# Kernel optimization log

Hardware: AMD Instinct MI355X
Metric: run time of the kernel (lower is better)

The kernel has to match this reference:

```python
import jax, jax.numpy as jnp
import numpy as np

B, R, F = 64, 196, 2048   # batch, regions, feature_dim
E, H, A = 512, 512, 512   # embed_dim, hidden_dim, attn_dim
V, L = 12000, 24          # vocab, seq_len


def setup_inputs() -> dict:
    key = jax.random.key(0)
    ks = jax.random.split(key, 16)
    s = lambda *d: 1.0 / np.sqrt(d[-1])
    inp = {
        'image_feats': jax.random.normal(ks[0], (B, R, F), jnp.float32),
        'caption_in': jax.random.randint(ks[1], (B, L), 0, V, jnp.int64),
        'emb_table': jax.random.normal(ks[2], (V, E), jnp.float32) * 0.02,
        'W_init_h': jax.random.normal(ks[3], (H, F), jnp.float32) * s(F),
        'b_init_h': jnp.zeros((H,), jnp.float32),
        'W_init_c': jax.random.normal(ks[4], (H, F), jnp.float32) * s(F),
        'b_init_c': jnp.zeros((H,), jnp.float32),
        'W_ih': jax.random.normal(ks[5], (4 * H, E + F), jnp.float32) * s(E + F),
        'b_ih': jnp.zeros((4 * H,), jnp.float32),
        'W_hh': jax.random.normal(ks[6], (4 * H, H), jnp.float32) * s(H),
        'b_hh': jnp.zeros((4 * H,), jnp.float32),
        'W_featp': jax.random.normal(ks[7], (A, F), jnp.float32) * s(F),
        'b_featp': jnp.zeros((A,), jnp.float32),
        'W_hidp': jax.random.normal(ks[8], (A, H), jnp.float32) * s(H),
        'b_hidp': jnp.zeros((A,), jnp.float32),
        'W_score': jax.random.normal(ks[9], (1, A), jnp.float32) * s(A),
        'b_score': jnp.zeros((1,), jnp.float32),
        'W_out': jax.random.normal(ks[10], (V, H), jnp.float32) * s(H),
        'b_out': jnp.zeros((V,), jnp.float32),
    }
    return inp


def _forward(image_feats, caption_in, emb_table, W_init_h, b_init_h, W_init_c,
             b_init_c, W_ih, b_ih, W_hh, b_hh, W_featp, b_featp, W_hidp,
             b_hidp, W_score, b_score, W_out, b_out):
    # init hidden state from mean image features
    mean_feats = image_feats.mean(axis=1)                      # (B, F)
    h0 = mean_feats @ W_init_h.T + b_init_h                    # (B, H)
    c0 = mean_feats @ W_init_c.T + b_init_c                    # (B, H)

    embeddings = emb_table[caption_in]                         # (B, L, E)  (dropout in eval mode = identity)

    # feature projection is constant over timesteps -> hoist out of the scan
    feat_proj = jnp.einsum('brf,af->bra', image_feats, W_featp) + b_featp  # (B, R, A)

    def step(carry, emb_t):
        h, c = carry
        # additive attention
        hid_proj = h @ W_hidp.T + b_hidp                       # (B, A)
        energy = jnp.tanh(feat_proj + hid_proj[:, None, :])    # (B, R, A)
        scores = jnp.einsum('bra,a->br', energy, W_score[0]) + b_score[0]
        alpha = jax.nn.softmax(scores, axis=1)                 # (B, R)
        context = jnp.einsum('br,brf->bf', alpha, image_feats) # (B, F)
        # LSTM cell (PyTorch gate order: i, f, g, o)
        x = jnp.concatenate([emb_t, context], axis=1)          # (B, E+F)
        gates = x @ W_ih.T + b_ih + h @ W_hh.T + b_hh          # (B, 4H)
        i, f, g, o = jnp.split(gates, 4, axis=1)
        c_new = jax.nn.sigmoid(f) * c + jax.nn.sigmoid(i) * jnp.tanh(g)
        h_new = jax.nn.sigmoid(o) * jnp.tanh(c_new)
        out = h_new @ W_out.T + b_out                          # (B, V)
        return (h_new, c_new), (out, alpha)

    emb_t = jnp.swapaxes(embeddings, 0, 1)                     # (L, B, E)
    _, (preds, alphas) = jax.lax.scan(step, (h0, c0), emb_t)
    predictions = jnp.swapaxes(preds, 0, 1)                    # (B, L, V)
    all_alphas = jnp.swapaxes(alphas, 0, 1)                    # (B, L, R)
    return predictions, all_alphas


def reference(image_feats, caption_in, emb_table, W_init_h, b_init_h, W_init_c,
              b_init_c, W_ih, b_ih, W_hh, b_hh, W_featp, b_featp, W_hidp,
              b_hidp, W_score, b_score, W_out, b_out):
    return _forward(image_feats, caption_in, emb_table, W_init_h, b_init_h,
                    W_init_c, b_init_c, W_ih, b_ih, W_hh, b_hh, W_featp,
                    b_featp, W_hidp, b_hidp, W_score, b_score, W_out, b_out)
```

## Files before the change

kernel.cpp:

```cpp
#include <hip/hip_runtime.h>

#define B_ 64
#define R_ 196
#define F_ 2048
#define E_ 512
#define H_ 512
#define A_ 512
#define V_ 12000
#define L_ 24

typedef __attribute__((ext_vector_type(8))) short bf16x8;
typedef __attribute__((ext_vector_type(4))) float f32x4;
typedef unsigned short ush;

__device__ __forceinline__ float fast_tanh(float x) {
    float t = __expf(2.f * x);
    return 1.f - 2.f / (t + 1.f);
}
__device__ __forceinline__ float fast_sig(float x) {
    return 1.f / (1.f + __expf(-x));
}
__device__ __forceinline__ ush f2bf(float x) {
    unsigned int u = __float_as_uint(x);
    return (ush)((u + 0x7fffu + ((u >> 16) & 1u)) >> 16);
}
__device__ __forceinline__ float bf2f(ush b) {
    return __uint_as_float(((unsigned int)b) << 16);
}

#define LROW 40

template<int SPLIT, int CMAP, bool NFAST>
__global__ __launch_bounds__(512) void gemm_big128(
    const ush* __restrict__ Ah, const ush* __restrict__ Al, int lda,
    const ush* __restrict__ Wh, const ush* __restrict__ Wl, int ldw,
    const float* __restrict__ bias, void* __restrict__ Cv,
    int ldc, int N, int K)
{
    constexpr int SMEM_BYTES = (SPLIT == 3) ? 61440 : 30720;
    __shared__ __align__(16) char smem[SMEM_BYTES];
    ush* sAh = (ush*)smem;
    ush* sBh = (ush*)(smem + 10240);
    ush* sAl = (ush*)(smem + 30720);
    ush* sBl = (ush*)(smem + 40960);

    const int tid = threadIdx.x;
    const int lane = tid & 63, w = tid >> 6;
    const int mw = w >> 2, nw = w & 3;

    const int nbx = gridDim.x, nby = gridDim.y;
    const int nwg = nbx * nby;
    const int orig = blockIdx.x + nbx * blockIdx.y;
    const int q = nwg >> 3, r = nwg & 7;
    const int xcd = orig & 7, idx = orig >> 3;
    const int lin = (xcd < r ? xcd * (q + 1) : r * (q + 1) + (xcd - r) * q) + idx;
    int bx, by;
    if constexpr (NFAST) { by = lin % nby; bx = lin / nby; }
    else                 { bx = lin % nbx; by = lin / nbx; }
    const int mtile = bx * 128;
    const int ntile = by * 256;

    const int fr = lane & 15, kg = (lane >> 4) * 8;
    const int arow = tid >> 2, aq = (tid & 3) * 8;

    f32x4 acc[4][4];
    #pragma unroll
    for (int mf = 0; mf < 4; ++mf)
        #pragma unroll
        for (int nf = 0; nf < 4; ++nf) acc[mf][nf] = {0.f, 0.f, 0.f, 0.f};

    const uint4 zv = make_uint4(0u, 0u, 0u, 0u);

    for (int kb = 0; kb < K; kb += 32) {
        uint4 a_h = *(const uint4*)(Ah + (size_t)(mtile + arow) * lda + kb + aq);
        uint4 a_l;
        uint4 b_h[2], b_l[2];
        #pragma unroll
        for (int p = 0; p < 2; ++p) {
            const int row = ntile + arow + 128 * p;
            b_h[p] = (row < N) ? *(const uint4*)(Wh + (size_t)row * ldw + kb + aq) : zv;
        }
        if constexpr (SPLIT == 3) {
            a_l = *(const uint4*)(Al + (size_t)(mtile + arow) * lda + kb + aq);
            #pragma unroll
            for (int p = 0; p < 2; ++p) {
                const int row = ntile + arow + 128 * p;
                b_l[p] = (row < N) ? *(const uint4*)(Wl + (size_t)row * ldw + kb + aq) : zv;
            }
        }

        __syncthreads();
        *(uint4*)(sAh + arow * LROW + aq) = a_h;
        #pragma unroll
        for (int p = 0; p < 2; ++p)
            *(uint4*)(sBh + (arow + 128 * p) * LROW + aq) = b_h[p];
        if constexpr (SPLIT == 3) {
            *(uint4*)(sAl + arow * LROW + aq) = a_l;
            #pragma unroll
            for (int p = 0; p < 2; ++p)
                *(uint4*)(sBl + (arow + 128 * p) * LROW + aq) = b_l[p];
        }
        __syncthreads();

        bf16x8 bh[4], bl[4];
        #pragma unroll
        for (int nf = 0; nf < 4; ++nf) {
            bh[nf] = *(const bf16x8*)(sBh + (nw * 64 + nf * 16 + fr) * LROW + kg);
            if constexpr (SPLIT == 3)
                bl[nf] = *(const bf16x8*)(sBl + (nw * 64 + nf * 16 + fr) * LROW + kg);
        }
        #pragma unroll
        for (int mf = 0; mf < 4; ++mf) {
            const bf16x8 ah = *(const bf16x8*)(sAh + (mw * 64 + mf * 16 + fr) * LROW + kg);
            if constexpr (SPLIT == 3) {
                const bf16x8 al = *(const bf16x8*)(sAl + (mw * 64 + mf * 16 + fr) * LROW + kg);
                #pragma unroll
                for (int nf = 0; nf < 4; ++nf) {
                    acc[mf][nf] = __builtin_amdgcn_mfma_f32_16x16x32_bf16(ah, bh[nf], acc[mf][nf], 0, 0, 0);
                    acc[mf][nf] = __builtin_amdgcn_mfma_f32_16x16x32_bf16(ah, bl[nf], acc[mf][nf], 0, 0, 0);
                    acc[mf][nf] = __builtin_amdgcn_mfma_f32_16x16x32_bf16(al, bh[nf], acc[mf][nf], 0, 0, 0);
                }
            } else {
                #pragma unroll
                for (int nf = 0; nf < 4; ++nf)
                    acc[mf][nf] = __builtin_amdgcn_mfma_f32_16x16x32_bf16(ah, bh[nf], acc[mf][nf], 0, 0, 0);
            }
        }
    }

    #pragma unroll
    for (int nf = 0; nf < 4; ++nf) {
        const int nn = ntile + nw * 64 + nf * 16 + fr;
        if (nn < N) {
            const float bv = bias ? bias[nn] : 0.f;
            #pragma unroll
            for (int mf = 0; mf < 4; ++mf) {
                #pragma unroll
                for (int rr = 0; rr < 4; ++rr) {
                    const int m = mtile + mw * 64 + mf * 16 + (lane >> 4) * 4 + rr;
                    const float v = acc[mf][nf][rr] + bv;
                    if constexpr (CMAP == 1)
                        ((ush*)Cv)[(size_t)m * ldc + nn] = f2bf(v);
                    else if constexpr (CMAP == 2) {
                        float* dst = (float*)Cv + (size_t)(m & 63) * (L_ * V_)
                                   + (size_t)(m >> 6) * V_ + nn;
                        __builtin_nontemporal_store(v, dst);
                    } else
                        ((float*)Cv)[(size_t)m * ldc + nn] = v;
                }
            }
        }
    }
}

template<int SPLIT, int CMAP, bool NFAST, int NF>
__global__ __launch_bounds__(256) void gemm_big(
    const ush* __restrict__ Ah, const ush* __restrict__ Al, int lda,
    const ush* __restrict__ Wh, const ush* __restrict__ Wl, int ldw,
    const float* __restrict__ bias, void* __restrict__ Cv,
    int ldc, int N, int K)
{
    constexpr int ABYTES = 64 * LROW * 2;
    constexpr int BBYTES = 64 * NF * LROW * 2;
    constexpr int SMEM_BYTES = (SPLIT == 3) ? 2 * (ABYTES + BBYTES) : (ABYTES + BBYTES);
    __shared__ __align__(16) char smem[SMEM_BYTES];
    ush* sAh = (ush*)smem;
    ush* sBh = (ush*)(smem + ABYTES);
    ush* sAl = (ush*)(smem + ABYTES + BBYTES);
    ush* sBl = (ush*)(smem + 2 * ABYTES + BBYTES);

    const int tid = threadIdx.x;
    const int lane = tid & 63, w = tid >> 6;

    const int nbx = gridDim.x, nby = gridDim.y;
    const int nwg = nbx * nby;
    int lin = blockIdx.x + nbx * blockIdx.y;
    if ((nwg & 7) == 0) {
        const int q = nwg >> 3;
        lin = (lin & 7) * q + (lin >> 3);
    }
    int bx, by;
    if constexpr (NFAST) { by = lin % nby; bx = lin / nby; }
    else                 { bx = lin % nbx; by = lin / nbx; }
    const int mtile = bx * 64;
    const int ntile = by * (64 * NF);

    const int fr = lane & 15, kg = (lane >> 4) * 8;
    const int arow = tid >> 2, aq = (tid & 3) * 8;

    f32x4 acc[4][NF];
    #pragma unroll
    for (int mf = 0; mf < 4; ++mf)
        #pragma unroll
        for (int nf = 0; nf < NF; ++nf) acc[mf][nf] = {0.f, 0.f, 0.f, 0.f};

    const uint4 zv = make_uint4(0u, 0u, 0u, 0u);

    for (int kb = 0; kb < K; kb += 32) {
        uint4 a_h = *(const uint4*)(Ah + (size_t)(mtile + arow) * lda + kb + aq);
        uint4 a_l;
        uint4 b_h[NF], b_l[NF];
        #pragma unroll
        for (int p = 0; p < NF; ++p) {
            const int row = ntile + arow + 64 * p;
            b_h[p] = (row < N) ? *(const uint4*)(Wh + (size_t)row * ldw + kb + aq) : zv;
        }
        if constexpr (SPLIT == 3) {
            a_l = *(const uint4*)(Al + (size_t)(mtile + arow) * lda + kb + aq);
            #pragma unroll
            for (int p = 0; p < NF; ++p) {
                const int row = ntile + arow + 64 * p;
                b_l[p] = (row < N) ? *(const uint4*)(Wl + (size_t)row * ldw + kb + aq) : zv;
            }
        }

        __syncthreads();
        *(uint4*)(sAh + arow * LROW + aq) = a_h;
        #pragma unroll
        for (int p = 0; p < NF; ++p)
            *(uint4*)(sBh + (arow + 64 * p) * LROW + aq) = b_h[p];
        if constexpr (SPLIT == 3) {
            *(uint4*)(sAl + arow * LROW + aq) = a_l;
            #pragma unroll
            for (int p = 0; p < NF; ++p)
                *(uint4*)(sBl + (arow + 64 * p) * LROW + aq) = b_l[p];
        }
        __syncthreads();

        bf16x8 bh[NF], bl[NF];
        #pragma unroll
        for (int nf = 0; nf < NF; ++nf) {
            bh[nf] = *(const bf16x8*)(sBh + (w * (16 * NF) + nf * 16 + fr) * LROW + kg);
            if constexpr (SPLIT == 3)
                bl[nf] = *(const bf16x8*)(sBl + (w * (16 * NF) + nf * 16 + fr) * LROW + kg);
        }
        #pragma unroll
        for (int mf = 0; mf < 4; ++mf) {
            const bf16x8 ah = *(const bf16x8*)(sAh + (mf * 16 + fr) * LROW + kg);
            if constexpr (SPLIT == 3) {
                const bf16x8 al = *(const bf16x8*)(sAl + (mf * 16 + fr) * LROW + kg);
                #pragma unroll
                for (int nf = 0; nf < NF; ++nf) {
                    acc[mf][nf] = __builtin_amdgcn_mfma_f32_16x16x32_bf16(ah, bh[nf], acc[mf][nf], 0, 0, 0);
                    acc[mf][nf] = __builtin_amdgcn_mfma_f32_16x16x32_bf16(ah, bl[nf], acc[mf][nf], 0, 0, 0);
                    acc[mf][nf] = __builtin_amdgcn_mfma_f32_16x16x32_bf16(al, bh[nf], acc[mf][nf], 0, 0, 0);
                }
            } else {
                #pragma unroll
                for (int nf = 0; nf < NF; ++nf)
                    acc[mf][nf] = __builtin_amdgcn_mfma_f32_16x16x32_bf16(ah, bh[nf], acc[mf][nf], 0, 0, 0);
            }
        }
    }

    #pragma unroll
    for (int nf = 0; nf < NF; ++nf) {
        const int nn = ntile + w * (16 * NF) + nf * 16 + fr;
        if (nn < N) {
            const float bv = bias ? bias[nn] : 0.f;
            #pragma unroll
            for (int mf = 0; mf < 4; ++mf) {
                #pragma unroll
                for (int rr = 0; rr < 4; ++rr) {
                    const int m = mtile + mf * 16 + (lane >> 4) * 4 + rr;
                    const float v = acc[mf][nf][rr] + bv;
                    if constexpr (CMAP == 1)
                        ((ush*)Cv)[(size_t)m * ldc + nn] = f2bf(v);
                    else
                        ((float*)Cv)[(size_t)m * ldc + nn] = v;
                }
            }
        }
    }
}

__global__ __launch_bounds__(256) void gemm_gates(
    const ush* __restrict__ Ah0, const ush* __restrict__ Al0, int lda0, int k0,
    const ush* __restrict__ Ah1, const ush* __restrict__ Al1, int lda1,
    const ush* __restrict__ Wh, const ush* __restrict__ Wl, int ldw,
    float* __restrict__ C, int ldc, long zstride, int kChunk)
{
    __shared__ ush sAh[64 * LROW];
    __shared__ ush sBh[64 * LROW];
    __shared__ ush sAl[64 * LROW];
    __shared__ ush sBl[64 * LROW];

    const int tid = threadIdx.x;
    const int ntile = blockIdx.x * 64;
    const int kStart = blockIdx.z * kChunk;
    const int lane = tid & 63, w = tid >> 6;
    const int lrow = tid >> 2;
    const int lcol = (tid & 3) * 8;
    const int nrow = ntile + lrow;

    f32x4 acc[4];
    #pragma unroll
    for (int f = 0; f < 4; ++f) acc[f] = {0.f, 0.f, 0.f, 0.f};

    const int fr = lane & 15;
    const int kg = (lane >> 4) * 8;

    for (int kb = kStart; kb < kStart + kChunk; kb += 32) {
        const ush *ph, *pl; int lda, loc;
        if (kb < k0) { ph = Ah0; pl = Al0; lda = lda0; loc = kb; }
        else         { ph = Ah1; pl = Al1; lda = lda1; loc = kb - k0; }

        uint4 a_h = *(const uint4*)(ph + (size_t)lrow * lda + loc + lcol);
        uint4 b_h = *(const uint4*)(Wh + (size_t)nrow * ldw + kb + lcol);
        uint4 a_l = *(const uint4*)(pl + (size_t)lrow * lda + loc + lcol);
        uint4 b_l = *(const uint4*)(Wl + (size_t)nrow * ldw + kb + lcol);

        __syncthreads();
        *(uint4*)(sAh + lrow * LROW + lcol) = a_h;
        *(uint4*)(sBh + lrow * LROW + lcol) = b_h;
        *(uint4*)(sAl + lrow * LROW + lcol) = a_l;
        *(uint4*)(sBl + lrow * LROW + lcol) = b_l;
        __syncthreads();

        const bf16x8 bh = *(const bf16x8*)(sBh + (16 * w + fr) * LROW + kg);
        const bf16x8 bl = *(const bf16x8*)(sBl + (16 * w + fr) * LROW + kg);

        #pragma unroll
        for (int f = 0; f < 4; ++f) {
            const bf16x8 ah = *(const bf16x8*)(sAh + (16 * f + fr) * LROW + kg);
            const bf16x8 al = *(const bf16x8*)(sAl + (16 * f + fr) * LROW + kg);
            acc[f] = __builtin_amdgcn_mfma_f32_16x16x32_bf16(ah, bh, acc[f], 0, 0, 0);
            acc[f] = __builtin_amdgcn_mfma_f32_16x16x32_bf16(ah, bl, acc[f], 0, 0, 0);
            acc[f] = __builtin_amdgcn_mfma_f32_16x16x32_bf16(al, bh, acc[f], 0, 0, 0);
        }
    }

    const int n = ntile + 16 * w + (lane & 15);
    float* Cz = C + (size_t)blockIdx.z * zstride;
    #pragma unroll
    for (int f = 0; f < 4; ++f)
        #pragma unroll
        for (int rr = 0; rr < 4; ++rr) {
            const int m = 16 * f + (lane >> 4) * 4 + rr;
            Cz[(size_t)m * ldc + n] = acc[f][rr];
        }
}

__global__ __launch_bounds__(256) void prep_feats(
    const float* __restrict__ feats, ush* __restrict__ fbh,
    ush* __restrict__ mh, ush* __restrict__ ml)
{
    const int fs = blockIdx.x;
    const int b  = blockIdx.y;
    const int f = fs * 512 + threadIdx.x * 2;
    const float2* fp = (const float2*)(feats + (size_t)b * R_ * F_ + f);
    ush* fo = fbh + (size_t)b * R_ * F_ + f;
    float sx = 0.f, sy = 0.f;
    for (int r = 0; r < R_; ++r) {
        const float2 v = fp[(size_t)r * (F_ / 2)];
        sx += v.x; sy += v.y;
        ushort2 u; u.x = f2bf(v.x); u.y = f2bf(v.y);
        *(ushort2*)(fo + (size_t)r * F_) = u;
    }
    const float s = 1.f / (float)R_;
    sx *= s; sy *= s;
    const size_t mi = (size_t)b * F_ + f;
    const ush hx = f2bf(sx); mh[mi] = hx;     ml[mi] = f2bf(sx - bf2f(hx));
    const ush hy = f2bf(sy); mh[mi + 1] = hy; ml[mi + 1] = f2bf(sy - bf2f(hy));
}

__global__ __launch_bounds__(256) void gather_split(
    const float* __restrict__ emb, const int* __restrict__ cap,
    ush* __restrict__ eh, ush* __restrict__ el)
{
    const int idx = blockIdx.x * 256 + threadIdx.x;
    const int bt = idx >> 7, j = idx & 127;
    const int tok = cap[bt];
    const float4 v = reinterpret_cast<const float4*>(emb)[(size_t)tok * (E_ / 4) + j];
    const float a[4] = {v.x, v.y, v.z, v.w};
    #pragma unroll
    for (int c = 0; c < 4; ++c) {
        const ush hi = f2bf(a[c]);
        eh[idx * 4 + c] = hi;
        el[idx * 4 + c] = f2bf(a[c] - bf2f(hi));
    }
}

__global__ __launch_bounds__(256) void split_kernel(
    const float* __restrict__ in, ush* __restrict__ hi, ush* __restrict__ lo, int n4)
{
    for (int i = blockIdx.x * 256 + threadIdx.x; i < n4; i += gridDim.x * 256) {
        const float4 v = reinterpret_cast<const float4*>(in)[i];
        const float a[4] = {v.x, v.y, v.z, v.w};
        #pragma unroll
        for (int c = 0; c < 4; ++c) {
            const ush h = f2bf(a[c]);
            hi[i * 4 + c] = h;
            if (lo) lo[i * 4 + c] = f2bf(a[c] - bf2f(h));
        }
    }
}

__global__ __launch_bounds__(256) void prep_wih(
    const float* __restrict__ W_ih, const float* __restrict__ W_hh,
    ush* __restrict__ wxh, ush* __restrict__ wxl,
    ush* __restrict__ wg2h, ush* __restrict__ wg2l)
{
    const int nrow = blockIdx.x;
    for (int k = threadIdx.x; k < E_; k += 256) {
        const float v = W_ih[(size_t)nrow * (E_ + F_) + k];
        const ush h = f2bf(v);
        wxh[(size_t)nrow * E_ + k] = h;
        wxl[(size_t)nrow * E_ + k] = f2bf(v - bf2f(h));
    }
    for (int k = threadIdx.x; k < F_ + H_; k += 256) {
        const float v = (k < F_) ? W_ih[(size_t)nrow * (E_ + F_) + E_ + k]
                                 : W_hh[(size_t)nrow * H_ + (k - F_)];
        const ush h = f2bf(v);
        wg2h[(size_t)nrow * (F_ + H_) + k] = h;
        wg2l[(size_t)nrow * (F_ + H_) + k] = f2bf(v - bf2f(h));
    }
}

__global__ __launch_bounds__(256) void transpose512(
    const float* __restrict__ in, float* __restrict__ out)
{
    const int idx = blockIdx.x * 256 + threadIdx.x;
    const int k = idx >> 9, a = idx & 511;
    out[idx] = in[(size_t)a * 512 + k];
    (void)k;
}

__global__ __launch_bounds__(256) void init_reduce(
    const float* __restrict__ initp, const float* __restrict__ b_init_h,
    const float* __restrict__ b_init_c, float* __restrict__ h0f,
    float* __restrict__ c, ush* __restrict__ h_hi, ush* __restrict__ h_lo)
{
    const int idx = blockIdx.x * 256 + threadIdx.x;
    const int b = idx >> 10, n = idx & 1023;
    float s = 0.f;
    #pragma unroll
    for (int z = 0; z < 8; ++z)
        s += initp[(size_t)z * (B_ * 1024) + (size_t)b * 1024 + n];
    if (n < 512) {
        s += b_init_h[n];
        h0f[b * H_ + n] = s;
        const ush hi = f2bf(s);
        h_hi[b * H_ + n] = hi;
        h_lo[b * H_ + n] = f2bf(s - bf2f(hi));
    } else {
        s += b_init_c[n - 512];
        c[b * H_ + (n - 512)] = s;
    }
}

template<bool ATT>
__global__ __launch_bounds__(512) void step_kernel(
    const float* __restrict__ gparts, const float* __restrict__ egates,
    const float* __restrict__ b_ih, const float* __restrict__ b_hh,
    float* __restrict__ c, const float* __restrict__ h0f,
    ush* __restrict__ h_hi, ush* __restrict__ h_lo,
    ush* __restrict__ hall_hi, ush* __restrict__ hall_lo,
    const float* __restrict__ whpT, const float* __restrict__ b_hidp,
    const ush* __restrict__ fpb, const float* __restrict__ W_score,
    const float* __restrict__ b_score,
    float* __restrict__ alpha, float* __restrict__ alph_out, int t)
{
    __shared__ float sh_h[H_];
    __shared__ float sh_hp[A_];
    __shared__ float sh_ws[A_];
    __shared__ float sh_sc[200];
    __shared__ float red[2];
    const int tid = threadIdx.x;
    const int b = blockIdx.x;
    const int n = tid;

    float hh;
    if (t > 0) {
        const float* eg = egates + ((size_t)b * L_ + (t - 1)) * 2048;
        float gi = b_ih[n] + b_hh[n] + eg[n];
        float gf = b_ih[n + 512] + b_hh[n + 512] + eg[n + 512];
        float gg = b_ih[n + 1024] + b_hh[n + 1024] + eg[n + 1024];
        float go = b_ih[n + 1536] + b_hh[n + 1536] + eg[n + 1536];
        #pragma unroll
        for (int z = 0; z < 8; ++z) {
            const float* gz = gparts + (size_t)z * B_ * 2048 + (size_t)b * 2048;
            gi += gz[n]; gf += gz[n + 512]; gg += gz[n + 1024]; go += gz[n + 1536];
        }
        const float cc = fast_sig(gf) * c[b * H_ + n] + fast_sig(gi) * fast_tanh(gg);
        hh = fast_sig(go) * fast_tanh(cc);
        c[b * H_ + n] = cc;
        const ush hi = f2bf(hh);
        const ush lo = f2bf(hh - bf2f(hi));
        h_hi[b * H_ + n] = hi;
        h_lo[b * H_ + n] = lo;
        const size_t hidx = ((size_t)(t - 1) * B_ + b) * H_ + n;
        hall_hi[hidx] = hi;
        hall_lo[hidx] = lo;
    } else {
        hh = h0f[b * H_ + n];
    }
    if constexpr (!ATT) return;

    sh_h[n] = hh;
    sh_ws[n] = W_score[n];
    __syncthreads();

    {
        float a0 = 0.f, a1 = 0.f, a2 = 0.f, a3 = 0.f;
        #pragma unroll 4
        for (int k = 0; k < H_; k += 4) {
            a0 = fmaf(sh_h[k + 0], whpT[(size_t)(k + 0) * A_ + tid], a0);
            a1 = fmaf(sh_h[k + 1], whpT[(size_t)(k + 1) * A_ + tid], a1);
            a2 = fmaf(sh_h[k + 2], whpT[(size_t)(k + 2) * A_ + tid], a2);
            a3 = fmaf(sh_h[k + 3], whpT[(size_t)(k + 3) * A_ + tid], a3);
        }
        sh_hp[tid] = (a0 + a1) + (a2 + a3) + b_hidp[tid];
    }
    __syncthreads();

    const int lane = tid & 63, wid = tid >> 6;
    for (int r = wid; r < R_; r += 8) {
        const ushort2* row = reinterpret_cast<const ushort2*>(fpb + ((size_t)b * R_ + r) * A_);
        float acc = 0.f;
        #pragma unroll
        for (int j = 0; j < 4; ++j) {
            const ushort2 u = row[lane + 64 * j];
            const int a = 2 * (lane + 64 * j);
            acc += fast_tanh(bf2f(u.x) + sh_hp[a]) * sh_ws[a];
            acc += fast_tanh(bf2f(u.y) + sh_hp[a + 1]) * sh_ws[a + 1];
        }
        for (int off = 32; off > 0; off >>= 1) acc += __shfl_down(acc, off);
        if (lane == 0) sh_sc[r] = acc + b_score[0];
    }
    __syncthreads();

    if (tid < 64) {
        float m = -1e30f;
        for (int r = tid; r < R_; r += 64) m = fmaxf(m, sh_sc[r]);
        for (int off = 32; off > 0; off >>= 1) m = fmaxf(m, __shfl_xor(m, off));
        float s = 0.f;
        for (int r = tid; r < R_; r += 64) s += __expf(sh_sc[r] - m);
        for (int off = 32; off > 0; off >>= 1) s += __shfl_xor(s, off);
        if (tid == 0) { red[0] = m; red[1] = 1.f / s; }
    }
    __syncthreads();
    const float m = red[0], is = red[1];
    if (tid < R_) {
        const float av = __expf(sh_sc[tid] - m) * is;
        alpha[b * R_ + tid] = av;
        alph_out[((size_t)b * L_ + t) * R_ + tid] = av;
    }
}

__global__ __launch_bounds__(256) void ctx_kernel(
    const ush* __restrict__ fbh, const float* __restrict__ alpha,
    ush* __restrict__ ctx_hi, ush* __restrict__ ctx_lo)
{
    __shared__ float sa[R_];
    const int tid = threadIdx.x;
    const int fs = blockIdx.x;
    const int b = blockIdx.y;
    if (tid < R_) sa[tid] = alpha[b * R_ + tid];
    __syncthreads();

    const int f0 = fs * 512 + tid * 2;
    const ush* fp = fbh + (size_t)b * R_ * F_ + f0;
    float cx = 0.f, cy = 0.f;
    #pragma unroll 4
    for (int r = 0; r < R_; ++r) {
        const float a = sa[r];
        const ushort2 u = *(const ushort2*)(fp + (size_t)r * F_);
        cx = fmaf(a, bf2f(u.x), cx); cy = fmaf(a, bf2f(u.y), cy);
    }
    const size_t ci = (size_t)b * F_ + f0;
    const ush hx = f2bf(cx);
    ctx_hi[ci] = hx; ctx_lo[ci] = f2bf(cx - bf2f(hx));
    const ush hy = f2bf(cy);
    ctx_hi[ci + 1] = hy; ctx_lo[ci + 1] = f2bf(cy - bf2f(hy));
}

extern "C" void kernel_launch(void* const* d_in, const int* in_sizes, int n_in,
                              void* d_out, int out_size, void* d_ws, size_t ws_size,
                              hipStream_t stream)
{
    const float* feats    = (const float*)d_in[0];
    const int*   cap      = (const int*)  d_in[1];
    const float* emb      = (const float*)d_in[2];
    const float* W_init_h = (const float*)d_in[3];
    const float* b_init_h = (const float*)d_in[4];
    const float* W_init_c = (const float*)d_in[5];
    const float* b_init_c = (const float*)d_in[6];
    const float* W_ih     = (const float*)d_in[7];
    const float* b_ih     = (const float*)d_in[8];
    const float* W_hh     = (const float*)d_in[9];
    const float* b_hh     = (const float*)d_in[10];
    const float* W_featp  = (const float*)d_in[11];
    const float* b_featp  = (const float*)d_in[12];
    const float* W_hidp   = (const float*)d_in[13];
    const float* b_hidp   = (const float*)d_in[14];
    const float* W_score  = (const float*)d_in[15];
    const float* b_score  = (const float*)d_in[16];
    const float* W_out    = (const float*)d_in[17];
    const float* b_out    = (const float*)d_in[18];

    float* pred     = (float*)d_out;
    float* alph_out = pred + (size_t)B_ * L_ * V_;

    char* p = (char*)d_ws;
    auto alloc = [&](size_t bytes) { char* q = p; p += (bytes + 255) & ~(size_t)255; return q; };

    ush*   fpb    = (ush*)  alloc((size_t)B_ * R_ * A_ * 2);
    ush*   eh     = (ush*)  alloc((size_t)B_ * L_ * E_ * 2);
    ush*   el     = (ush*)  alloc((size_t)B_ * L_ * E_ * 2);
    ush*   mh     = (ush*)  alloc((size_t)B_ * F_ * 2);
    ush*   ml     = (ush*)  alloc((size_t)B_ * F_ * 2);
    ush*   fbh    = (ush*)  alloc((size_t)B_ * R_ * F_ * 2);
    ush*   wfp_h  = (ush*)  alloc((size_t)A_ * F_ * 2);
    ush*   wiH    = (ush*)  alloc((size_t)1024 * F_ * 2);
    ush*   wiL    = (ush*)  alloc((size_t)1024 * F_ * 2);
    ush*   wxh    = (ush*)  alloc((size_t)2048 * E_ * 2);
    ush*   wxl    = (ush*)  alloc((size_t)2048 * E_ * 2);
    ush*   wg2h   = (ush*)  alloc((size_t)2048 * (F_ + H_) * 2);
    ush*   wg2l   = (ush*)  alloc((size_t)2048 * (F_ + H_) * 2);
    ush*   woh    = (ush*)  alloc((size_t)V_ * H_ * 2);
    ush*   wol    = (ush*)  alloc((size_t)V_ * H_ * 2);
    float* whpT   = (float*)alloc((size_t)H_ * A_ * 4);
    float* egates = (float*)alloc((size_t)B_ * L_ * 2048 * 4);
    float* h0f    = (float*)alloc((size_t)B_ * H_ * 4);
    float* c      = (float*)alloc((size_t)B_ * H_ * 4);
    ush*   h_hi   = (ush*)  alloc((size_t)B_ * H_ * 2);
    ush*   h_lo   = (ush*)  alloc((size_t)B_ * H_ * 2);
    ush*   hallh  = (ush*)  alloc((size_t)L_ * B_ * H_ * 2);
    ush*   halll  = (ush*)  alloc((size_t)L_ * B_ * H_ * 2);
    ush*   ctx_hi = (ush*)  alloc((size_t)B_ * F_ * 2);
    ush*   ctx_lo = (ush*)  alloc((size_t)B_ * F_ * 2);
    float* alpha  = (float*)alloc((size_t)B_ * R_ * 4);
    float* gparts = (float*)alloc((size_t)8 * B_ * 2048 * 4);
    float* initp  = (float*)alloc((size_t)8 * B_ * 1024 * 4);

    prep_feats<<<dim3(4, B_), 256, 0, stream>>>(feats, fbh, mh, ml);
    gather_split<<<768, 256, 0, stream>>>(emb, cap, eh, el);
    split_kernel<<<2048, 256, 0, stream>>>(W_out, woh, wol, V_ * H_ / 4);
    split_kernel<<<512, 256, 0, stream>>>(W_init_h, wiH, wiL, H_ * F_ / 4);
    split_kernel<<<512, 256, 0, stream>>>(W_init_c, wiH + (size_t)512 * F_,
                                          wiL + (size_t)512 * F_, H_ * F_ / 4);
    split_kernel<<<512, 256, 0, stream>>>(W_featp, wfp_h, nullptr, A_ * F_ / 4);
    prep_wih<<<2048, 256, 0, stream>>>(W_ih, W_hh, wxh, wxl, wg2h, wg2l);
    transpose512<<<1024, 256, 0, stream>>>(W_hidp, whpT);

    gemm_gates<<<dim3(16, 1, 8), 256, 0, stream>>>(
        mh, ml, F_, F_,
        mh, ml, F_,
        wiH, wiL, F_,
        initp, 1024, (long)B_ * 1024, F_ / 8);
    init_reduce<<<256, 256, 0, stream>>>(initp, b_init_h, b_init_c, h0f, c, h_hi, h_lo);

    gemm_big<1, 1, true, 2><<<dim3(196, 4), 256, 0, stream>>>(
        fbh, nullptr, F_, wfp_h, nullptr, F_, b_featp, fpb, A_, A_, F_);

    gemm_big<3, 0, false, 2><<<dim3(24, 16), 256, 0, stream>>>(
        eh, el, E_, wxh, wxl, E_, nullptr, egates, 2048, 2048, E_);

    for (int t = 0; t < L_; ++t) {
        step_kernel<true><<<B_, 512, 0, stream>>>(
            gparts, egates, b_ih, b_hh, c, h0f, h_hi, h_lo, hallh, halll,
            whpT, b_hidp, fpb, W_score, b_score, alpha, alph_out, t);

        ctx_kernel<<<dim3(4, B_), 256, 0, stream>>>(fbh, alpha, ctx_hi, ctx_lo);

        gemm_gates<<<dim3(32, 1, 8), 256, 0, stream>>>(
            ctx_hi, ctx_lo, F_, F_,
            h_hi, h_lo, H_,
            wg2h, wg2l, F_ + H_,
            gparts, 4 * H_, (long)B_ * 4 * H_, (F_ + H_) / 8);
    }

    step_kernel<false><<<B_, 512, 0, stream>>>(
        gparts, egates, b_ih, b_hh, c, h0f, h_hi, h_lo, hallh, halll,
        whpT, b_hidp, fpb, W_score, b_score, alpha, alph_out, L_);

    gemm_big128<3, 2, false><<<dim3(12, 47), 512, 0, stream>>>(
        hallh, halll, H_, woh, wol, H_, b_out, pred, 0, V_, H_);
}
```

Baseline: 2.100 ms.

## Fuse attention step and context reduction into one per-batch kernel

Merges the per-timestep attention/LSTM-update kernel with the context-weighted-sum kernel, launching 4 blocks per batch that each redundantly compute the LSTM cell and attention softmax and then reduce one 512-wide feature slice. The cell state is double-buffered so the redundant blocks do not race on it. The hidden-projection weight is stored as bf16 to halve its reads. A template argument of the feature-projection GEMM launch also changes along with its grid. This removes one launch per timestep and the alpha round trip through global memory, at the cost of 4x redundant attention work per batch.

```diff
diff --git a/kernel.cpp b/kernel.cpp
--- a/kernel.cpp
+++ b/kernel.cpp
@@ -418,18 +418,17 @@
 }
 
 __global__ __launch_bounds__(256) void transpose512(
-    const float* __restrict__ in, float* __restrict__ out)
+    const float* __restrict__ in, ush* __restrict__ out)
 {
     const int idx = blockIdx.x * 256 + threadIdx.x;
     const int k = idx >> 9, a = idx & 511;
-    out[idx] = in[(size_t)a * 512 + k];
-    (void)k;
+    out[idx] = f2bf(in[(size_t)a * 512 + k]);
 }
 
 __global__ __launch_bounds__(256) void init_reduce(
     const float* __restrict__ initp, const float* __restrict__ b_init_h,
     const float* __restrict__ b_init_c, float* __restrict__ h0f,
-    float* __restrict__ c, ush* __restrict__ h_hi, ush* __restrict__ h_lo)
+    float* __restrict__ c0, ush* __restrict__ h_hi, ush* __restrict__ h_lo)
 {
     const int idx = blockIdx.x * 256 + threadIdx.x;
     const int b = idx >> 10, n = idx & 1023;
@@ -445,21 +444,22 @@
         h_lo[b * H_ + n] = f2bf(s - bf2f(hi));
     } else {
         s += b_init_c[n - 512];
-        c[b * H_ + (n - 512)] = s;
+        c0[b * H_ + (n - 512)] = s;
     }
 }
 
 template<bool ATT>
-__global__ __launch_bounds__(512) void step_kernel(
+__global__ __launch_bounds__(512) void step2_kernel(
     const float* __restrict__ gparts, const float* __restrict__ egates,
     const float* __restrict__ b_ih, const float* __restrict__ b_hh,
-    float* __restrict__ c, const float* __restrict__ h0f,
+    float* __restrict__ c2, const float* __restrict__ h0f,
     ush* __restrict__ h_hi, ush* __restrict__ h_lo,
     ush* __restrict__ hall_hi, ush* __restrict__ hall_lo,
-    const float* __restrict__ whpT, const float* __restrict__ b_hidp,
+    const ush* __restrict__ whpT, const float* __restrict__ b_hidp,
     const ush* __restrict__ fpb, const float* __restrict__ W_score,
-    const float* __restrict__ b_score,
-    float* __restrict__ alpha, float* __restrict__ alph_out, int t)
+    const float* __restrict__ b_score, const ush* __restrict__ fbh,
+    ush* __restrict__ ctx_hi, ush* __restrict__ ctx_lo,
+    float* __restrict__ alph_out, int t)
 {
     __shared__ float sh_h[H_];
     __shared__ float sh_hp[A_];
@@ -467,11 +467,14 @@
     __shared__ float sh_sc[200];
     __shared__ float red[2];
     const int tid = threadIdx.x;
-    const int b = blockIdx.x;
+    const int fs = blockIdx.x;
+    const int b = blockIdx.y;
     const int n = tid;
 
     float hh;
     if (t > 0) {
+        const float* c_old = c2 + (size_t)((t - 1) & 1) * B_ * H_;
+        float* c_new = c2 + (size_t)(t & 1) * B_ * H_;
         const float* eg = egates + ((size_t)b * L_ + (t - 1)) * 2048;
         float gi = b_ih[n] + b_hh[n] + eg[n];
         float gf = b_ih[n + 512] + b_hh[n + 512] + eg[n + 512];
@@ -482,16 +485,18 @@
             const float* gz = gparts + (size_t)z * B_ * 2048 + (size_t)b * 2048;
             gi += gz[n]; gf += gz[n + 512]; gg += gz[n + 1024]; go += gz[n + 1536];
         }
-        const float cc = fast_sig(gf) * c[b * H_ + n] + fast_sig(gi) * fast_tanh(gg);
+        const float cc = fast_sig(gf) * c_old[b * H_ + n] + fast_sig(gi) * fast_tanh(gg);
         hh = fast_sig(go) * fast_tanh(cc);
-        c[b * H_ + n] = cc;
-        const ush hi = f2bf(hh);
-        const ush lo = f2bf(hh - bf2f(hi));
-        h_hi[b * H_ + n] = hi;
-        h_lo[b * H_ + n] = lo;
-        const size_t hidx = ((size_t)(t - 1) * B_ + b) * H_ + n;
-        hall_hi[hidx] = hi;
-        hall_lo[hidx] = lo;
+        if (fs == 0) {
+            c_new[b * H_ + n] = cc;
+            const ush hi = f2bf(hh);
+            const ush lo = f2bf(hh - bf2f(hi));
+            h_hi[b * H_ + n] = hi;
+            h_lo[b * H_ + n] = lo;
+            const size_t hidx = ((size_t)(t - 1) * B_ + b) * H_ + n;
+            hall_hi[hidx] = hi;
+            hall_lo[hidx] = lo;
+        }
     } else {
         hh = h0f[b * H_ + n];
     }
@@ -505,10 +510,10 @@
         float a0 = 0.f, a1 = 0.f, a2 = 0.f, a3 = 0.f;
         #pragma unroll 4
         for (int k = 0; k < H_; k += 4) {
-            a0 = fmaf(sh_h[k + 0], whpT[(size_t)(k + 0) * A_ + tid], a0);
-            a1 = fmaf(sh_h[k + 1], whpT[(size_t)(k + 1) * A_ + tid], a1);
-            a2 = fmaf(sh_h[k + 2], whpT[(size_t)(k + 2) * A_ + tid], a2);
-            a3 = fmaf(sh_h[k + 3], whpT[(size_t)(k + 3) * A_ + tid], a3);
+            a0 = fmaf(sh_h[k + 0], bf2f(whpT[(size_t)(k + 0) * A_ + tid]), a0);
+            a1 = fmaf(sh_h[k + 1], bf2f(whpT[(size_t)(k + 1) * A_ + tid]), a1);
+            a2 = fmaf(sh_h[k + 2], bf2f(whpT[(size_t)(k + 2) * A_ + tid]), a2);
+            a3 = fmaf(sh_h[k + 3], bf2f(whpT[(size_t)(k + 3) * A_ + tid]), a3);
         }
         sh_hp[tid] = (a0 + a1) + (a2 + a3) + b_hidp[tid];
     }
@@ -543,36 +548,23 @@
     const float m = red[0], is = red[1];
     if (tid < R_) {
         const float av = __expf(sh_sc[tid] - m) * is;
-        alpha[b * R_ + tid] = av;
-        alph_out[((size_t)b * L_ + t) * R_ + tid] = av;
-    }
-}
-
-__global__ __launch_bounds__(256) void ctx_kernel(
-    const ush* __restrict__ fbh, const float* __restrict__ alpha,
-    ush* __restrict__ ctx_hi, ush* __restrict__ ctx_lo)
-{
-    __shared__ float sa[R_];
-    const int tid = threadIdx.x;
-    const int fs = blockIdx.x;
-    const int b = blockIdx.y;
-    if (tid < R_) sa[tid] = alpha[b * R_ + tid];
+        sh_sc[tid] = av;
+        if (fs == 0) alph_out[((size_t)b * L_ + t) * R_ + tid] = av;
+    }
     __syncthreads();
 
-    const int f0 = fs * 512 + tid * 2;
-    const ush* fp = fbh + (size_t)b * R_ * F_ + f0;
-    float cx = 0.f, cy = 0.f;
-    #pragma unroll 4
-    for (int r = 0; r < R_; ++r) {
-        const float a = sa[r];
-        const ushort2 u = *(const ushort2*)(fp + (size_t)r * F_);
-        cx = fmaf(a, bf2f(u.x), cx); cy = fmaf(a, bf2f(u.y), cy);
-    }
-    const size_t ci = (size_t)b * F_ + f0;
-    const ush hx = f2bf(cx);
-    ctx_hi[ci] = hx; ctx_lo[ci] = f2bf(cx - bf2f(hx));
-    const ush hy = f2bf(cy);
-    ctx_hi[ci + 1] = hy; ctx_lo[ci + 1] = f2bf(cy - bf2f(hy));
+    {
+        const int f0 = fs * 512 + tid;
+        const ush* fp2 = fbh + (size_t)b * R_ * F_ + f0;
+        float cx = 0.f;
+        #pragma unroll 4
+        for (int r = 0; r < R_; ++r)
+            cx = fmaf(sh_sc[r], bf2f(fp2[(size_t)r * F_]), cx);
+        const size_t ci = (size_t)b * F_ + f0;
+        const ush hx = f2bf(cx);
+        ctx_hi[ci] = hx;
+        ctx_lo[ci] = f2bf(cx - bf2f(hx));
+    }
 }
 
 extern "C" void kernel_launch(void* const* d_in, const int* in_sizes, int n_in,
@@ -620,17 +612,16 @@
     ush*   wg2l   = (ush*)  alloc((size_t)2048 * (F_ + H_) * 2);
     ush*   woh    = (ush*)  alloc((size_t)V_ * H_ * 2);
     ush*   wol    = (ush*)  alloc((size_t)V_ * H_ * 2);
-    float* whpT   = (float*)alloc((size_t)H_ * A_ * 4);
+    ush*   whpT   = (ush*)  alloc((size_t)H_ * A_ * 2);
     float* egates = (float*)alloc((size_t)B_ * L_ * 2048 * 4);
     float* h0f    = (float*)alloc((size_t)B_ * H_ * 4);
-    float* c      = (float*)alloc((size_t)B_ * H_ * 4);
+    float* c2     = (float*)alloc((size_t)2 * B_ * H_ * 4);
     ush*   h_hi   = (ush*)  alloc((size_t)B_ * H_ * 2);
     ush*   h_lo   = (ush*)  alloc((size_t)B_ * H_ * 2);
     ush*   hallh  = (ush*)  alloc((size_t)L_ * B_ * H_ * 2);
     ush*   halll  = (ush*)  alloc((size_t)L_ * B_ * H_ * 2);
     ush*   ctx_hi = (ush*)  alloc((size_t)B_ * F_ * 2);
     ush*   ctx_lo = (ush*)  alloc((size_t)B_ * F_ * 2);
-    float* alpha  = (float*)alloc((size_t)B_ * R_ * 4);
     float* gparts = (float*)alloc((size_t)8 * B_ * 2048 * 4);
     float* initp  = (float*)alloc((size_t)8 * B_ * 1024 * 4);
 
@@ -649,20 +640,19 @@
         mh, ml, F_,
         wiH, wiL, F_,
         initp, 1024, (long)B_ * 1024, F_ / 8);
-    init_reduce<<<256, 256, 0, stream>>>(initp, b_init_h, b_init_c, h0f, c, h_hi, h_lo);
-
-    gemm_big<1, 1, true, 2><<<dim3(196, 4), 256, 0, stream>>>(
+    init_reduce<<<256, 256, 0, stream>>>(initp, b_init_h, b_init_c, h0f, c2, h_hi, h_lo);
+
+    gemm_big<1, 1, true, 1><<<dim3(196, 8), 256, 0, stream>>>(
         fbh, nullptr, F_, wfp_h, nullptr, F_, b_featp, fpb, A_, A_, F_);
 
     gemm_big<3, 0, false, 2><<<dim3(24, 16), 256, 0, stream>>>(
         eh, el, E_, wxh, wxl, E_, nullptr, egates, 2048, 2048, E_);
 
     for (int t = 0; t < L_; ++t) {
-        step_kernel<true><<<B_, 512, 0, stream>>>(
-            gparts, egates, b_ih, b_hh, c, h0f, h_hi, h_lo, hallh, halll,
-            whpT, b_hidp, fpb, W_score, b_score, alpha, alph_out, t);
-
-        ctx_kernel<<<dim3(4, B_), 256, 0, stream>>>(fbh, alpha, ctx_hi, ctx_lo);
+        step2_kernel<true><<<dim3(4, B_), 512, 0, stream>>>(
+            gparts, egates, b_ih, b_hh, c2, h0f, h_hi, h_lo, hallh, halll,
+            whpT, b_hidp, fpb, W_score, b_score, fbh, ctx_hi, ctx_lo,
+            alph_out, t);
 
         gemm_gates<<<dim3(32, 1, 8), 256, 0, stream>>>(
             ctx_hi, ctx_lo, F_, F_,
@@ -671,9 +661,10 @@
             gparts, 4 * H_, (long)B_ * 4 * H_, (F_ + H_) / 8);
     }
 
-    step_kernel<false><<<B_, 512, 0, stream>>>(
-        gparts, egates, b_ih, b_hh, c, h0f, h_hi, h_lo, hallh, halll,
-        whpT, b_hidp, fpb, W_score, b_score, alpha, alph_out, L_);
+    step2_kernel<false><<<dim3(1, B_), 512, 0, stream>>>(
+        gparts, egates, b_ih, b_hh, c2, h0f, h_hi, h_lo, hallh, halll,
+        whpT, b_hidp, fpb, W_score, b_score, fbh, ctx_hi, ctx_lo,
+        alph_out, L_);
 
     gemm_big128<3, 2, false><<<dim3(12, 47), 512, 0, stream>>>(
         hallh, halll, H_, woh, wol, H_, b_out, pred, 0, V_, H_);
```

After: 1.961 ms, median of 2. 6.6% less time.
